# Kernel optimization log

Hardware: AMD Instinct MI355X
Metric: run time of the kernel (lower is better)

Reference implementation:

```python
import jax, jax.numpy as jnp
import numpy as np

B, S = 4, 1024
D_MODEL, N_HEADS, D_SPACE = 1024, 16, 128
N_QK, N_V, N_KNOW = 4096, 4096, 8192
NC_QK, NC_V, NC_KNOW = 64, 64, 64
KC_QK, KC_V, KC_KNOW = 8, 8, 8
MAX_K = 128


def _unit_rows(key, shape):
    w = jax.random.normal(key, shape, jnp.float32)
    return w / (jnp.linalg.norm(w, axis=-1, keepdims=True) + 1e-8)


def setup_inputs() -> dict:
    key = jax.random.key(0)
    ks = jax.random.split(key, 16)
    sd = 0.02
    return {
        "x": jax.random.normal(ks[0], (B, S, D_MODEL), jnp.float32),
        "neuron_emb": jax.random.normal(ks[1], (N_QK + N_V + N_KNOW, D_SPACE), jnp.float32) * sd,
        "proj_attn_k": jax.random.normal(ks[2], (D_MODEL, 3 * D_SPACE), jnp.float32) * sd,
        "proj_attn_b": jnp.zeros((3 * D_SPACE,), jnp.float32),
        "tau_attn_k": jax.random.normal(ks[3], (D_MODEL, 3), jnp.float32) * sd,
        "tau_attn_b": jnp.zeros((3,), jnp.float32),
        "proj_know_k": jax.random.normal(ks[4], (D_MODEL, D_SPACE), jnp.float32) * sd,
        "proj_know_b": jnp.zeros((D_SPACE,), jnp.float32),
        "tau_know_k": jax.random.normal(ks[5], (D_MODEL, 1), jnp.float32) * sd,
        "tau_know_b": jnp.zeros((1,), jnp.float32),
        "cluster_emb_qk": jax.random.normal(ks[6], (NC_QK, D_SPACE), jnp.float32) * sd,
        "cluster_emb_v": jax.random.normal(ks[7], (NC_V, D_SPACE), jnp.float32) * sd,
        "cluster_emb_know": jax.random.normal(ks[8], (NC_KNOW, D_SPACE), jnp.float32) * sd,
        "qk_neurons": _unit_rows(ks[9], (N_QK, D_MODEL)),
        "v_neurons": _unit_rows(ks[10], (N_V, D_MODEL)),
        "know_neurons": _unit_rows(ks[11], (N_KNOW, D_MODEL)),
        "expand_O": jax.random.normal(ks[12], (D_MODEL, D_MODEL), jnp.float32) * sd,
        "ln1_scale": jnp.ones((D_MODEL,), jnp.float32),
        "ln1_bias": jnp.zeros((D_MODEL,), jnp.float32),
        "ln2_scale": jnp.ones((D_MODEL,), jnp.float32),
        "ln2_bias": jnp.zeros((D_MODEL,), jnp.float32),
    }


def _layer_norm(x, scale, bias, eps=1e-6):
    mean = jnp.mean(x, axis=-1, keepdims=True)
    var = jnp.mean(jnp.square(x - mean), axis=-1, keepdims=True)
    return (x - mean) / jnp.sqrt(var + eps) * scale + bias


@jax.checkpoint
def sense_emit(x, neurons, gates):
    # x:[B,S,D] neurons:[N,D] gates:[B,S,N] -> [B,S,D]
    activations = jnp.einsum('bsd,nd->bsn', x, neurons)
    return jnp.einsum('bsn,nd->bsd', activations * gates, neurons)


def threshold_gate(scores, tau, max_k):
    raw_gate = scores - tau
    gate = jnp.where(raw_gate > 0, raw_gate, 1e-8 * jnp.exp(raw_gate))
    exp_gate = jnp.exp(gate) - 1.0
    topk_vals, _ = jax.lax.top_k(exp_gate, max_k)
    threshold = topk_vals[:, :, -1:]
    exp_gate = jnp.where(exp_gate >= threshold, exp_gate, 0.0)
    gate_sum = exp_gate.sum(axis=-1, keepdims=True) + 1e-8
    gate_strength = jnp.tanh(exp_gate.max(axis=-1, keepdims=True))
    return exp_gate / gate_sum * gate_strength


def hierarchical_gate(h, neuron_emb, cluster_emb, tau, n_neurons, n_clusters, k_cluster, max_k):
    Bb, Ss, _ = h.shape
    cluster_size = n_neurons // n_clusters
    ce = cluster_emb / (jnp.linalg.norm(cluster_emb, axis=-1, keepdims=True) + 1e-8)
    cluster_scores = jnp.einsum('bsd,cd->bsc', h, ce)
    _, topk_ids = jax.lax.top_k(cluster_scores, k_cluster)
    cluster_probs = jax.nn.softmax(cluster_scores, axis=-1)
    cluster_freq = cluster_probs.mean(axis=(0, 1))
    cluster_aux = ((cluster_freq - 1.0 / n_clusters) ** 2).sum() * n_clusters
    active_ids = (topk_ids * cluster_size)[:, :, :, None] + jnp.arange(cluster_size)[None, None, None, :]
    active_ids = active_ids.reshape(Bb, Ss, k_cluster * cluster_size)
    active_emb = neuron_emb[active_ids]  # [B,S,A,d_space]
    active_scores = jnp.einsum('bsd,bsnd->bsn', h, active_emb)
    active_gates = threshold_gate(active_scores, tau, max_k)
    gates = jnp.zeros((Bb, Ss, n_neurons), active_gates.dtype)
    bi = jnp.arange(Bb)[:, None, None]
    si = jnp.arange(Ss)[None, :, None]
    gates = gates.at[bi, si, active_ids].set(active_gates)
    neuron_freq = gates.mean(axis=(0, 1))
    neuron_aux = ((neuron_freq - 1.0 / n_neurons) ** 2).sum() * n_neurons
    return gates, cluster_aux, neuron_aux


def _forward(x, neuron_emb, proj_attn_k, proj_attn_b, tau_attn_k, tau_attn_b,
             proj_know_k, proj_know_b, tau_know_k, tau_know_b,
             cluster_emb_qk, cluster_emb_v, cluster_emb_know,
             qk_neurons, v_neurons, know_neurons, expand_O,
             ln1_scale, ln1_bias, ln2_scale, ln2_bias):
    emb_norm = neuron_emb / (jnp.linalg.norm(neuron_emb, axis=-1, keepdims=True) + 1e-8)
    qk_emb = emb_norm[:N_QK]
    v_emb = emb_norm[N_QK:N_QK + N_V]
    know_emb = emb_norm[N_QK + N_V:]

    # --- attention circuit (pre-LN) ---
    h1 = _layer_norm(x, ln1_scale, ln1_bias)
    h_all = h1 @ proj_attn_k + proj_attn_b
    h_Q, h_K, h_V = jnp.split(h_all, 3, axis=-1)
    tau_all = h1 @ tau_attn_k + tau_attn_b
    gate_Q, cq, nq = hierarchical_gate(h_Q, qk_emb, cluster_emb_qk, tau_all[:, :, 0:1], N_QK, NC_QK, KC_QK, MAX_K)
    gate_K, ck, nk = hierarchical_gate(h_K, qk_emb, cluster_emb_qk, tau_all[:, :, 1:2], N_QK, NC_QK, KC_QK, MAX_K)
    gate_V, cv, nv = hierarchical_gate(h_V, v_emb, cluster_emb_v, tau_all[:, :, 2:3], N_V, NC_V, KC_V, MAX_K)
    aux = cq + ck + cv + nq + nk + nv

    Q = sense_emit(h1, qk_neurons, gate_Q)
    K = sense_emit(h1, qk_neurons, gate_K)
    V = sense_emit(h1, v_neurons, gate_V)
    d_head = D_MODEL // N_HEADS
    Q = Q.reshape(B, S, N_HEADS, d_head).transpose(0, 2, 1, 3)
    K = K.reshape(B, S, N_HEADS, d_head).transpose(0, 2, 1, 3)
    V = V.reshape(B, S, N_HEADS, d_head).transpose(0, 2, 1, 3)
    scores = jnp.einsum('bhsd,bhtd->bhst', Q, K) / jnp.sqrt(jnp.float32(d_head))
    causal = jnp.tril(jnp.ones((S, S), dtype=jnp.bool_))
    scores = jnp.where(causal, scores, jnp.finfo(scores.dtype).min)
    attn_w = jax.nn.softmax(scores, axis=-1)
    attn_out = jnp.einsum('bhst,bhtd->bhsd', attn_w, V)
    attn_out = attn_out.transpose(0, 2, 1, 3).reshape(B, S, D_MODEL) @ expand_O
    x = x + attn_out

    # --- knowledge circuit (pre-LN) ---
    h2 = _layer_norm(x, ln2_scale, ln2_bias)
    h_know = h2 @ proj_know_k + proj_know_b
    tau_know = h2 @ tau_know_k + tau_know_b
    gate_know, caux_k2, naux_k2 = hierarchical_gate(h_know, know_emb, cluster_emb_know, tau_know, N_KNOW, NC_KNOW, KC_KNOW, MAX_K)
    aux = aux + caux_k2 + naux_k2
    know_out = sense_emit(h2, know_neurons, gate_know)
    x = x + know_out
    return x, aux


def reference(x, neuron_emb, proj_attn_k, proj_attn_b, tau_attn_k, tau_attn_b,
              proj_know_k, proj_know_b, tau_know_k, tau_know_b,
              cluster_emb_qk, cluster_emb_v, cluster_emb_know,
              qk_neurons, v_neurons, know_neurons, expand_O,
              ln1_scale, ln1_bias, ln2_scale, ln2_bias):
    return _forward(x, neuron_emb, proj_attn_k, proj_attn_b, tau_attn_k, tau_attn_b,
                    proj_know_k, proj_know_b, tau_know_k, tau_know_b,
                    cluster_emb_qk, cluster_emb_v, cluster_emb_know,
                    qk_neurons, v_neurons, know_neurons, expand_O,
                    ln1_scale, ln1_bias, ln2_scale, ln2_bias)
```

## Files before the change

### kernel.cpp

```cpp
#include <hip/hip_runtime.h>

typedef unsigned short u16;
typedef unsigned int u32;
typedef unsigned long long u64;
typedef __attribute__((ext_vector_type(8))) short s16x8;
typedef __attribute__((ext_vector_type(4))) float f32x4;
typedef __attribute__((ext_vector_type(16))) float f32x16;

#define NTOK 4096
#define CAP 144

#define MFMA32(a,b,c) __builtin_amdgcn_mfma_f32_32x32x16_bf16(a,b,c,0,0,0)
#define MFMA16(a,b,c) __builtin_amdgcn_mfma_f32_16x16x32_bf16(a,b,c,0,0,0)

union U16x8 { uint4 u; u16 s[8]; };
union Dw4 { u32 d[4]; s16x8 v; };

__device__ __forceinline__ u16 f2bf(float f) {
    u32 u = __float_as_uint(f);
    u32 r = u + 0x7FFFu + ((u >> 16) & 1u);
    return (u16)(r >> 16);
}
__device__ __forceinline__ u32 pkbf(float lo, float hi) {
    u32 r;
    asm("v_cvt_pk_bf16_f32 %0, %1, %2" : "=v"(r) : "v"(lo), "v"(hi));
    return r;
}
__device__ __forceinline__ u32 mapkey(float f) {
    u32 b = __float_as_uint(f);
    return (b & 0x80000000u) ? ~b : (b | 0x80000000u);
}

__global__ __launch_bounds__(256) void norm_rows_kernel(const float* __restrict__ in,
                                                        u16* __restrict__ out16,
                                                        float* __restrict__ outRow, int rows)
{
    int row = blockIdx.x * 4 + (threadIdx.x >> 6);
    int lane = threadIdx.x & 63;
    if (row >= rows) return;
    float2 v = *(const float2*)&in[(size_t)row * 128 + lane * 2];
    float ss = v.x * v.x + v.y * v.y;
    #pragma unroll
    for (int o = 1; o < 64; o <<= 1) ss += __shfl_xor(ss, o);
    float rn = 1.0f / (sqrtf(ss) + 1e-8f);
    float2 ov = make_float2(v.x * rn, v.y * rn);
    if (out16)
        *(u32*)&out16[(size_t)row * 128 + lane * 2] = pkbf(ov.x, ov.y);
    if (outRow)
        *(float2*)&outRow[(size_t)row * 128 + lane * 2] = ov;
}

__global__ __launch_bounds__(256) void cast_bf16_kernel(const float* __restrict__ in,
                                                        u16* __restrict__ out, int n)
{
    int i = (blockIdx.x * 256 + threadIdx.x) * 4;
    if (i >= n) return;
    float4 v = *(const float4*)&in[i];
    ushort4 o;
    o.x = f2bf(v.x); o.y = f2bf(v.y); o.z = f2bf(v.z); o.w = f2bf(v.w);
    *(ushort4*)&out[i] = o;
}

__global__ __launch_bounds__(256) void cast_gateh_kernel(const float* __restrict__ h, int stride,
                                                         int ngates, u16* __restrict__ out)
{
    int t = blockIdx.x, tid = threadIdx.x;
    int total = ngates * 128;
    for (int i = tid; i < total; i += 256) {
        int g = i >> 7, d = i & 127;
        out[(size_t)g * NTOK * 128 + (size_t)t * 128 + d] = f2bf(h[(size_t)t * stride + i]);
    }
}

__global__ void transpose_cast_kernel(const float* __restrict__ in, u16* __restrict__ out,
                                      int Nn, int Kk)
{
    __shared__ float sT[64][65];
    int n0 = blockIdx.x * 64, k0 = blockIdx.y * 64;
    int tx = threadIdx.x, ty = threadIdx.y;
    #pragma unroll
    for (int r = 0; r < 64; r += 4)
        sT[ty + r][tx] = in[(size_t)(k0 + ty + r) * Nn + n0 + tx];
    __syncthreads();
    #pragma unroll
    for (int r = 0; r < 64; r += 4)
        out[(size_t)(n0 + ty + r) * Kk + k0 + tx] = f2bf(sT[tx][ty + r]);
}

__global__ void ntab_transpose_kernel(const u16* __restrict__ in, u16* __restrict__ out, int NCLv)
{
    __shared__ u16 tile[64][65];
    int cc = blockIdx.x, db = blockIdx.y * 64, jb = blockIdx.z * 64;
    int tx = threadIdx.x, ty = threadIdx.y;
    const u16* src = in + (size_t)cc * NCLv * 1024;
    #pragma unroll
    for (int r = 0; r < 64; r += 4)
        tile[ty + r][tx] = src[(size_t)(jb + ty + r) * 1024 + db + tx];
    __syncthreads();
    u16* dst = out + (size_t)cc * NCLv * 1024;
    #pragma unroll
    for (int r = 0; r < 64; r += 4)
        dst[(size_t)(db + ty + r) * NCLv + jb + tx] = tile[tx][ty + r];
}

__global__ __launch_bounds__(256) void ln_kernel(const float* __restrict__ x,
                                                 const float* __restrict__ gam,
                                                 const float* __restrict__ bet,
                                                 float* __restrict__ out,
                                                 u16* __restrict__ outbf)
{
    __shared__ float red[8];
    int t = blockIdx.x, tid = threadIdx.x;
    const float* row = x + (size_t)t * 1024;
    float4 v = *(const float4*)&row[tid * 4];
    float s = v.x + v.y + v.z + v.w;
    #pragma unroll
    for (int o = 1; o < 64; o <<= 1) s += __shfl_xor(s, o);
    if ((tid & 63) == 0) red[tid >> 6] = s;
    __syncthreads();
    float mean = (red[0] + red[1] + red[2] + red[3]) * (1.0f / 1024.0f);
    float d0 = v.x - mean, d1 = v.y - mean, d2 = v.z - mean, d3 = v.w - mean;
    float ss = d0 * d0 + d1 * d1 + d2 * d2 + d3 * d3;
    #pragma unroll
    for (int o = 1; o < 64; o <<= 1) ss += __shfl_xor(ss, o);
    if ((tid & 63) == 0) red[4 + (tid >> 6)] = ss;
    __syncthreads();
    float var = (red[4] + red[5] + red[6] + red[7]) * (1.0f / 1024.0f);
    float rstd = 1.0f / sqrtf(var + 1e-6f);
    int d = tid * 4;
    float4 g4 = *(const float4*)&gam[d];
    float4 b4 = *(const float4*)&bet[d];
    float4 o4;
    o4.x = d0 * rstd * g4.x + b4.x;
    o4.y = d1 * rstd * g4.y + b4.y;
    o4.z = d2 * rstd * g4.z + b4.z;
    o4.w = d3 * rstd * g4.w + b4.w;
    *(float4*)&out[(size_t)t * 1024 + d] = o4;
    if (outbf) {
        ushort4 ob;
        ob.x = f2bf(o4.x); ob.y = f2bf(o4.y); ob.z = f2bf(o4.z); ob.w = f2bf(o4.w);
        *(ushort4*)&outbf[(size_t)t * 1024 + d] = ob;
    }
}

__global__ __launch_bounds__(256) void gemm_mfma_kernel(const u16* __restrict__ A,
                                                        const u16* __restrict__ Bt,
                                                        const float* __restrict__ bias,
                                                        const float* __restrict__ resid,
                                                        float* __restrict__ C, int N, int K)
{
    __shared__ __align__(16) u16 sA[128 * 80];
    __shared__ __align__(16) u16 sB[128 * 80];
    int n0 = blockIdx.x * 128, m0 = blockIdx.y * 128;
    int tid = threadIdx.x;
    int l = tid & 63, wid = tid >> 6;
    int wm = wid >> 1, wn = wid & 1;
    int l15 = l & 15, hi4 = l >> 4;
    f32x4 acc[4][4];
    #pragma unroll
    for (int i = 0; i < 4; ++i)
        #pragma unroll
        for (int j = 0; j < 4; ++j)
            #pragma unroll
            for (int q = 0; q < 4; ++q) acc[i][j][q] = 0.f;

    int sr = tid >> 1, scb = (tid & 1) * 4;
    for (int k0 = 0; k0 < K; k0 += 64) {
        __syncthreads();
        #pragma unroll
        for (int j = 0; j < 4; ++j) {
            int ch = scb + j;
            uint4 va = *(const uint4*)&A[(size_t)(m0 + sr) * K + k0 + ch * 8];
            *(uint4*)&sA[sr * 80 + ch * 8] = va;
            uint4 vb = *(const uint4*)&Bt[(size_t)(n0 + sr) * K + k0 + ch * 8];
            *(uint4*)&sB[sr * 80 + ch * 8] = vb;
        }
        __syncthreads();
        #pragma unroll
        for (int kc = 0; kc < 2; ++kc) {
            s16x8 af[4], bf[4];
            #pragma unroll
            for (int mf = 0; mf < 4; ++mf)
                af[mf] = *(const s16x8*)&sA[(wm * 64 + mf * 16 + l15) * 80 + kc * 32 + hi4 * 8];
            #pragma unroll
            for (int nf = 0; nf < 4; ++nf)
                bf[nf] = *(const s16x8*)&sB[(wn * 64 + nf * 16 + l15) * 80 + kc * 32 + hi4 * 8];
            #pragma unroll
            for (int mf = 0; mf < 4; ++mf)
                #pragma unroll
                for (int nf = 0; nf < 4; ++nf)
                    acc[mf][nf] = MFMA16(af[mf], bf[nf], acc[mf][nf]);
        }
    }
    #pragma unroll
    for (int mf = 0; mf < 4; ++mf)
        #pragma unroll
        for (int nf = 0; nf < 4; ++nf)
            #pragma unroll
            for (int j = 0; j < 4; ++j) {
                int row = m0 + wm * 64 + mf * 16 + hi4 * 4 + j;
                int col = n0 + wn * 64 + nf * 16 + l15;
                float v = acc[mf][nf][j];
                if (bias) v += bias[col];
                if (resid) v += resid[(size_t)row * N + col];
                C[(size_t)row * N + col] = v;
            }
}

__global__ __launch_bounds__(64) void vecproj_kernel(const float* __restrict__ h,
                                                     const float* __restrict__ W,
                                                     const float* __restrict__ bias,
                                                     float* __restrict__ out, int nw)
{
    int t = blockIdx.x, lane = threadIdx.x;
    float p0 = 0.f, p1 = 0.f, p2 = 0.f;
    #pragma unroll
    for (int it = 0; it < 4; ++it) {
        int d = it * 256 + lane * 4;
        float4 h4 = *(const float4*)&h[(size_t)t * 1024 + d];
        if (nw == 1) {
            float4 w4 = *(const float4*)&W[d];
            p0 += h4.x * w4.x + h4.y * w4.y + h4.z * w4.z + h4.w * w4.w;
        } else {
            float4 w0 = *(const float4*)&W[d * 3];
            float4 w1 = *(const float4*)&W[d * 3 + 4];
            float4 w2 = *(const float4*)&W[d * 3 + 8];
            p0 += h4.x * w0.x + h4.y * w0.w + h4.z * w1.z + h4.w * w2.y;
            p1 += h4.x * w0.y + h4.y * w1.x + h4.z * w1.w + h4.w * w2.z;
            p2 += h4.x * w0.z + h4.y * w1.y + h4.z * w2.x + h4.w * w2.w;
        }
    }
    #pragma unroll
    for (int o = 1; o < 64; o <<= 1) {
        p0 += __shfl_xor(p0, o);
        p1 += __shfl_xor(p1, o);
        p2 += __shfl_xor(p2, o);
    }
    if (lane == 0) {
        out[(size_t)t * nw + 0] = p0 + bias[0];
        if (nw > 1) out[(size_t)t * nw + 1] = p1 + bias[1];
        if (nw > 2) out[(size_t)t * nw + 2] = p2 + bias[2];
    }
}

__global__ __launch_bounds__(256) void cluster_kernel(
    const float* __restrict__ hsrc, int hstride,
    const float* __restrict__ cebase,
    float* __restrict__ cprob, int* __restrict__ topcg, int gate_base)
{
    __shared__ float sH[32 * 136];
    __shared__ float sC[64 * 136];
    int gy = blockIdx.y;
    const float* ce = cebase + (size_t)(gy >> 1) * (64 * 128);
    int hoff = gy * 128;
    int gout = gate_base + gy;
    int t0 = blockIdx.x * 32;
    int tid = threadIdx.x;

    {
        int r = tid >> 3, c0 = (tid & 7) * 16;
        const float* src = hsrc + (size_t)(t0 + r) * hstride + hoff + c0;
        #pragma unroll
        for (int q = 0; q < 16; q += 4)
            *(float4*)&sH[r * 136 + c0 + q] = *(const float4*)&src[q];
    }
    {
        int r = tid >> 2, c0 = (tid & 3) * 32;
        const float* src = ce + (size_t)r * 128 + c0;
        #pragma unroll
        for (int q = 0; q < 32; q += 4)
            *(float4*)&sC[r * 136 + c0 + q] = *(const float4*)&src[q];
    }
    __syncthreads();

    int tt = tid >> 3, cl0 = tid & 7;
    float acc[8] = {};
    for (int d4 = 0; d4 < 128; d4 += 4) {
        float4 hv = *(const float4*)&sH[tt * 136 + d4];
        #pragma unroll
        for (int c8 = 0; c8 < 8; ++c8) {
            float4 cv = *(const float4*)&sC[(cl0 + 8 * c8) * 136 + d4];
            acc[c8] = fmaf(hv.x, cv.x, acc[c8]);
            acc[c8] = fmaf(hv.y, cv.y, acc[c8]);
            acc[c8] = fmaf(hv.z, cv.z, acc[c8]);
            acc[c8] = fmaf(hv.w, cv.w, acc[c8]);
        }
    }
    __syncthreads();
    float* sS = sH;
    #pragma unroll
    for (int c8 = 0; c8 < 8; ++c8)
        sS[tt * 72 + cl0 + 8 * c8] = acc[c8];
    __syncthreads();

    int w = tid >> 6, lane = tid & 63;
    for (int k = 0; k < 8; ++k) {
        int t = w * 8 + k;
        float s = sS[t * 72 + lane];
        float mx = s;
        #pragma unroll
        for (int o = 1; o < 64; o <<= 1) mx = fmaxf(mx, __shfl_xor(mx, o));
        float e = expf(s - mx);
        float sm = e;
        #pragma unroll
        for (int o = 1; o < 64; o <<= 1) sm += __shfl_xor(sm, o);
        cprob[((size_t)gout * NTOK + t0 + t) * 64 + lane] = e / sm;
        int rank = 0;
        for (int j = 0; j < 64; ++j) {
            float sj = sS[t * 72 + j];
            rank += (sj > s || (sj == s && j < lane)) ? 1 : 0;
        }
        if (rank < 8) topcg[((size_t)gout * NTOK + t0 + t) * 8 + rank] = lane;
    }
}

__global__ __launch_bounds__(1024) void listbuild_kernel(
    const int* __restrict__ topc_base, u32* __restrict__ entries_base,
    u32* __restrict__ tiletab_base, int* __restrict__ ntiles_base)
{
    __shared__ int cnt[64], offp[64], woff[64], tbase[64];
    int g = blockIdx.x;
    const int* tc = topc_base + (size_t)g * NTOK * 8;
    u32* eg = entries_base + (size_t)g * 40960;
    u32* tt = tiletab_base + (size_t)g * 640;
    int tid = threadIdx.x;
    if (tid < 64) { cnt[tid] = 0; woff[tid] = 0; }
    __syncthreads();
    int myc[32];
    #pragma unroll
    for (int i = 0; i < 32; ++i) {
        int t = tid * 4 + (i >> 3), s = i & 7;
        int c = tc[(size_t)t * 8 + s] & 63;
        myc[i] = c;
        atomicAdd(&cnt[c], 1);
    }
    __syncthreads();
    if (tid < 64) {
        int pc = (cnt[tid] + 63) & ~63;
        int sum = pc;
        #pragma unroll
        for (int o = 1; o < 64; o <<= 1) { int up = __shfl_up(sum, o); if (tid >= o) sum += up; }
        offp[tid] = sum - pc;
        int nt = pc >> 6;
        int tsum = nt;
        #pragma unroll
        for (int o = 1; o < 64; o <<= 1) { int up = __shfl_up(tsum, o); if (tid >= o) tsum += up; }
        tbase[tid] = tsum - nt;
        if (tid == 63) ntiles_base[g] = tsum;
    }
    __syncthreads();
    int totpad = offp[63] + ((cnt[63] + 63) & ~63);
    for (int i = tid; i < totpad; i += 1024) eg[i] = 0xFFFFFFFFu;
    __syncthreads();
    #pragma unroll
    for (int i = 0; i < 32; ++i) {
        int t = tid * 4 + (i >> 3), s = i & 7;
        int c = myc[i];
        int pos = offp[c] + atomicAdd(&woff[c], 1);
        eg[pos] = (u32)t | ((u32)s << 12);
    }
    __syncthreads();
    if (tid < 64) {
        int nt = ((cnt[tid] + 63) & ~63) >> 6;
        int eb = offp[tid] >> 6;
        for (int k2 = 0; k2 < nt; ++k2)
            tt[tbase[tid] + k2] = ((u32)tid << 16) | (u32)(eb + k2);
    }
}

template<int NCL>
__global__ __launch_bounds__(256) void score_bs_kernel(
    const u16* __restrict__ hgbf,
    const u16* __restrict__ embbase,
    float* __restrict__ scsbase,
    const u32* __restrict__ entries,
    const u32* __restrict__ tiletab,
    const int* __restrict__ ntiles)
{
    constexpr int NFR = NCL / 16;
    __shared__ __align__(16) u16 sH[64 * 136];
    __shared__ __align__(16) u16 sE[NCL * 136];
    __shared__ u32 ent[64];
    int gy = blockIdx.y;
    int bsw = ((int)blockIdx.x & 7) * 80 + ((int)blockIdx.x >> 3);
    if (bsw >= ntiles[gy]) return;
    u32 te = tiletab[(size_t)gy * 640 + bsw];
    int c = (int)(te >> 16) & 63;
    int e0 = (int)(te & 0x3FFu) * 64;
    const u32* eg = entries + (size_t)gy * 40960;
    const u16* Hg = hgbf + (size_t)gy * NTOK * 128;
    const u16* emb = embbase + (size_t)(gy >> 1) * 4096 * 128 + (size_t)c * NCL * 128;
    float* scs = scsbase + (size_t)gy * NTOK * (8 * NCL);

    int tid = threadIdx.x;
    int w = tid >> 6, lane = tid & 63;
    int l15 = lane & 15, hi4 = lane >> 4;

    if (tid < 64) ent[tid] = eg[e0 + tid];
    __syncthreads();

    #pragma unroll
    for (int u = 0; u < 4; ++u) {
        int idx = tid + u * 256;
        int r = idx >> 4, cq = idx & 15;
        int t = (int)(ent[r] & 4095u);
        uint4 v = *(const uint4*)&Hg[(size_t)t * 128 + cq * 8];
        *(uint4*)&sH[r * 136 + cq * 8] = v;
    }
    #pragma unroll
    for (int u = 0; u < NCL / 16; ++u) {
        int idx = tid + u * 256;
        int r = idx >> 4, cq = idx & 15;
        uint4 v = *(const uint4*)&emb[(size_t)r * 128 + cq * 8];
        *(uint4*)&sE[r * 136 + cq * 8] = v;
    }
    __syncthreads();

    f32x4 acc[NFR];
    #pragma unroll
    for (int nf = 0; nf < NFR; ++nf) { acc[nf][0] = 0.f; acc[nf][1] = 0.f; acc[nf][2] = 0.f; acc[nf][3] = 0.f; }
    #pragma unroll
    for (int kc = 0; kc < 4; ++kc) {
        s16x8 af = *(const s16x8*)&sH[(w * 16 + l15) * 136 + kc * 32 + hi4 * 8];
        #pragma unroll
        for (int nf = 0; nf < NFR; ++nf) {
            s16x8 bf = *(const s16x8*)&sE[(nf * 16 + l15) * 136 + kc * 32 + hi4 * 8];
            acc[nf] = MFMA16(af, bf, acc[nf]);
        }
    }

    int row0 = w * 16 + hi4 * 4;
    #pragma unroll
    for (int jj = 0; jj < 4; ++jj) {
        u32 e = ent[row0 + jj];
        if (e != 0xFFFFFFFFu) {
            int t = (int)(e & 4095u), s = (int)((e >> 12) & 7u);
            float* orow = scs + (size_t)t * (8 * NCL) + s * NCL;
            #pragma unroll
            for (int nf = 0; nf < NFR; ++nf)
                orow[nf * 16 + l15] = acc[nf][jj];
        }
    }
}

template<int NCAND, int LGCS>
__global__ __launch_bounds__(256) void gate_select_kernel(
    float* __restrict__ scsg,
    const float* __restrict__ tausrc, int taustride,
    const int* __restrict__ topcg,
    int* __restrict__ gidx, float* __restrict__ gval, int* __restrict__ gcnt,
    int gate_base)
{
    constexpr int CSM = (1 << LGCS) - 1;
    __shared__ float lds_scs[4][NCAND];
    __shared__ int   lds_hist[4][256];
    __shared__ int   lds_topc[4][8];
    __shared__ float lds_keg[4][CAP];

    int gy = blockIdx.y;
    int gg = gate_base + gy;
    int tauoff = gy;
    const int* tsrc = topcg + (size_t)gg * NTOK * 8;
    float* scs = scsg + (size_t)gy * NTOK * NCAND;
    gidx += (size_t)gg * NTOK * CAP;
    gval += (size_t)gg * NTOK * CAP;
    gcnt += gg * NTOK;

    int w = threadIdx.x >> 6, lane = threadIdx.x & 63;
    int t = blockIdx.x * 4 + w;

    float* srow = scs + (size_t)t * NCAND;
    #pragma unroll
    for (int c0 = 0; c0 < NCAND; c0 += 64)
        lds_scs[w][c0 + lane] = srow[c0 + lane];
    if (lane < 8) lds_topc[w][lane] = tsrc[(size_t)t * 8 + lane] & 63;

    unsigned prefix = 0; int k = 128;
    #pragma unroll
    for (int shift = 24; shift >= 0; shift -= 8) {
        lds_hist[w][lane] = 0;
        lds_hist[w][lane + 64] = 0;
        lds_hist[w][lane + 128] = 0;
        lds_hist[w][lane + 192] = 0;
        unsigned mhi = (shift == 24) ? 0u : (0xFFFFFFFFu << (shift + 8));
        #pragma unroll
        for (int ii = 0; ii < NCAND; ii += 64) {
            unsigned key = mapkey(lds_scs[w][ii + lane]);
            if ((key & mhi) == prefix) atomicAdd(&lds_hist[w][(key >> shift) & 255], 1);
        }
        int s0 = lds_hist[w][4 * lane], s1 = lds_hist[w][4 * lane + 1];
        int s2 = lds_hist[w][4 * lane + 2], s3 = lds_hist[w][4 * lane + 3];
        int sl = s0 + s1 + s2 + s3;
        int suf = sl;
        #pragma unroll
        for (int o = 1; o < 64; o <<= 1) {
            int ov = __shfl_down(suf, o);
            if (lane + o < 64) suf += ov;
        }
        int run = suf - sl;
        int seld = -1, selk = 0;
        if (run < k && k <= run + s3) { seld = 4 * lane + 3; selk = k - run; }
        run += s3;
        if (seld < 0 && run < k && k <= run + s2) { seld = 4 * lane + 2; selk = k - run; }
        run += s2;
        if (seld < 0 && run < k && k <= run + s1) { seld = 4 * lane + 1; selk = k - run; }
        run += s1;
        if (seld < 0 && run < k && k <= run + s0) { seld = 4 * lane + 0; selk = k - run; }
        u64 mk = __ballot(seld >= 0);
        int owner = __ffsll(mk) - 1;
        int sd = __shfl(seld, owner);
        k = __shfl(selk, owner);
        prefix |= ((unsigned)sd) << shift;
    }
    unsigned thrkey = prefix;

    float tau = tausrc[(size_t)t * taustride + tauoff];
    int basec = 0;
    float lsum = 0.f, lmaxs = -3.0e38f;
    #pragma unroll
    for (int c0 = 0; c0 < NCAND; c0 += 64) {
        float s = lds_scs[w][c0 + lane];
        lmaxs = fmaxf(lmaxs, s);
        bool pred = (mapkey(s) >= thrkey);
        float eg = 0.f;
        if (pred) {
            float raw = s - tau;
            float g2 = raw > 0.f ? raw : 1e-8f * expf(raw);
            eg = expf(g2) - 1.0f;
            lsum += eg;
        }
        u64 mk = __ballot(pred);
        int pos = basec + __popcll(mk & ((1ull << lane) - 1ull));
        if (pred && pos < CAP) {
            lds_hist[w][pos] = c0 + lane;
            lds_keg[w][pos] = eg;
        }
        basec += __popcll(mk);
    }
    #pragma unroll
    for (int o = 1; o < 64; o <<= 1) {
        lsum += __shfl_xor(lsum, o);
        lmaxs = fmaxf(lmaxs, __shfl_xor(lmaxs, o));
    }
    float rawm = lmaxs - tau;
    float gm = rawm > 0.f ? rawm : 1e-8f * expf(rawm);
    float egm = expf(gm) - 1.0f;
    float scalev = tanhf(egm) / (lsum + 1e-8f);
    int nkept = basec < CAP ? basec : CAP;

    for (int p = lane; p < nkept; p += 64) {
        int i = lds_hist[w][p];
        float eg = lds_keg[w][p];
        int neuron = (lds_topc[w][i >> LGCS] << LGCS) + (i & CSM);
        gidx[(size_t)t * CAP + p] = neuron;
        gval[(size_t)t * CAP + p] = eg * scalev;
    }
    if (lane == 0) gcnt[t] = nkept;

    #pragma unroll
    for (int c0 = 0; c0 < NCAND; c0 += 64) {
        int i = c0 + lane;
        float s = lds_scs[w][i];
        float wv = 0.f;
        if (mapkey(s) >= thrkey) {
            float raw = s - tau;
            float g2 = raw > 0.f ? raw : 1e-8f * expf(raw);
            wv = (expf(g2) - 1.0f) * scalev;
        }
        srow[i] = wv;
    }
}

template<int NCL>
__global__ __launch_bounds__(256) void sense_bs_kernel(
    const u16* __restrict__ hbf,
    const u16* __restrict__ ntab,
    const u16* __restrict__ ntabT,
    const float* __restrict__ Wg,
    const u32* __restrict__ entries,
    const u32* __restrict__ tiletab,
    const int* __restrict__ ntiles,
    u16* __restrict__ partial)
{
    constexpr int NTP = NCL + 8;
    constexpr int NFR = NCL / 16;
    constexpr int LQ = (NCL == 64) ? 3 : 4;
    __shared__ __align__(16) char smem[(64 + NCL) * 144 + NCL * 128 + 256];
    u16* sH = (u16*)smem;
    u16* sN = (u16*)(smem + 64 * 144);
    u16* sNT = (u16*)smem;
    u16* sP = (u16*)(smem + (64 + NCL) * 144);
    u32* ent = (u32*)(smem + (64 + NCL) * 144 + NCL * 128);

    int bsw = ((int)blockIdx.x & 7) * 80 + ((int)blockIdx.x >> 3);
    if (bsw >= *ntiles) return;
    u32 te = tiletab[bsw];
    int c = (int)(te >> 16) & 63;
    int e0 = (int)(te & 0x3FFu) * 64;

    int tid = threadIdx.x;
    int w = tid >> 6, lane = tid & 63;
    int l15 = lane & 15, hi4 = lane >> 4;

    if (tid < 64) ent[tid] = entries[e0 + tid];
    __syncthreads();

    const u16* nbase = ntab + (size_t)c * NCL * 1024;
    const u16* ntT = ntabT + (size_t)c * NCL * 1024;

    f32x4 acc[NFR];
    #pragma unroll
    for (int nf = 0; nf < NFR; ++nf) { acc[nf][0] = 0.f; acc[nf][1] = 0.f; acc[nf][2] = 0.f; acc[nf][3] = 0.f; }

    for (int k0 = 0; k0 < 1024; k0 += 64) {
        __syncthreads();
        #pragma unroll
        for (int u = 0; u < 2; ++u) {
            int idx = tid + u * 256;
            int r = idx >> 3, cq = idx & 7;
            int t = (int)(ent[r] & 4095u);
            uint4 v = *(const uint4*)&hbf[(size_t)t * 1024 + k0 + cq * 8];
            *(uint4*)&sH[r * 72 + cq * 8] = v;
        }
        #pragma unroll
        for (int u = 0; u < NCL / 32; ++u) {
            int idx = tid + u * 256;
            int r = idx >> 3, cq = idx & 7;
            uint4 v = *(const uint4*)&nbase[(size_t)r * 1024 + k0 + cq * 8];
            *(uint4*)&sN[r * 72 + cq * 8] = v;
        }
        __syncthreads();
        #pragma unroll
        for (int kc = 0; kc < 2; ++kc) {
            s16x8 af = *(const s16x8*)&sH[(w * 16 + l15) * 72 + kc * 32 + hi4 * 8];
            #pragma unroll
            for (int nf = 0; nf < NFR; ++nf) {
                s16x8 bf = *(const s16x8*)&sN[(nf * 16 + l15) * 72 + kc * 32 + hi4 * 8];
                acc[nf] = MFMA16(af, bf, acc[nf]);
            }
        }
    }
    __syncthreads();

    int row0 = w * 16 + hi4 * 4;
    u32 erow[4]; bool evalid[4];
    #pragma unroll
    for (int jj = 0; jj < 4; ++jj) { erow[jj] = ent[row0 + jj]; evalid[jj] = (erow[jj] != 0xFFFFFFFFu); }
    #pragma unroll
    for (int jj = 0; jj < 4; ++jj) {
        int t = (int)(erow[jj] & 4095u), s = (int)((erow[jj] >> 12) & 7u);
        const float* wrow = Wg + (size_t)t * (8 * NCL) + s * NCL;
        #pragma unroll
        for (int nf = 0; nf < NFR; ++nf) {
            float wv = wrow[nf * 16 + l15];
            sP[(row0 + jj) * NCL + nf * 16 + l15] = f2bf(acc[nf][jj] * wv);
        }
    }
    __syncthreads();

    for (int dch = 0; dch < 16; ++dch) {
        int d0 = dch * 64;
        __syncthreads();
        #pragma unroll
        for (int u = 0; u < NCL / 32; ++u) {
            int v = tid + u * 256;
            int dr = v >> LQ, jq = v & ((1 << LQ) - 1);
            uint4 t4 = *(const uint4*)&ntT[(size_t)(d0 + dr) * NCL + jq * 8];
            *(uint4*)&sNT[dr * NTP + jq * 8] = t4;
        }
        __syncthreads();
        f32x4 ab[4];
        #pragma unroll
        for (int df = 0; df < 4; ++df) { ab[df][0] = 0.f; ab[df][1] = 0.f; ab[df][2] = 0.f; ab[df][3] = 0.f; }
        #pragma unroll
        for (int kc = 0; kc < NCL / 32; ++kc) {
            s16x8 af = *(const s16x8*)&sP[(w * 16 + l15) * NCL + kc * 32 + hi4 * 8];
            #pragma unroll
            for (int df = 0; df < 4; ++df) {
                s16x8 bf = *(const s16x8*)&sNT[(df * 16 + l15) * NTP + kc * 32 + hi4 * 8];
                ab[df] = MFMA16(af, bf, ab[df]);
            }
        }
        #pragma unroll
        for (int jj = 0; jj < 4; ++jj) {
            if (evalid[jj]) {
                int t = (int)(erow[jj] & 4095u), s = (int)((erow[jj] >> 12) & 7u);
                u16* prow = partial + ((size_t)t * 8 + s) * 1024 + d0;
                #pragma unroll
                for (int df = 0; df < 4; ++df)
                    prow[df * 16 + l15] = f2bf(ab[df][jj]);
            }
        }
    }
}

__global__ __launch_bounds__(256) void slot_reduce_kernel(
    const u16* __restrict__ partial, u16* __restrict__ outq, float* __restrict__ outadd)
{
    int t = blockIdx.x, tid = threadIdx.x;
    int d0 = tid * 4;
    float s0 = 0.f, s1 = 0.f, s2 = 0.f, s3 = 0.f;
    #pragma unroll
    for (int s = 0; s < 8; ++s) {
        ushort4 u = *(const ushort4*)&partial[((size_t)t * 8 + s) * 1024 + d0];
        s0 += __uint_as_float((u32)u.x << 16);
        s1 += __uint_as_float((u32)u.y << 16);
        s2 += __uint_as_float((u32)u.z << 16);
        s3 += __uint_as_float((u32)u.w << 16);
    }
    if (outq) {
        int b = t >> 10, st = t & 1023;
        int head = d0 >> 6, dh = d0 & 63;
        ushort4 o;
        o.x = f2bf(s0); o.y = f2bf(s1); o.z = f2bf(s2); o.w = f2bf(s3);
        *(ushort4*)&outq[(((size_t)b * 16 + head) * 1024 + st) * 64 + dh] = o;
    } else {
        float* op = outadd + (size_t)t * 1024 + d0;
        float4 cur = *(const float4*)op;
        cur.x += s0; cur.y += s1; cur.z += s2; cur.w += s3;
        *(float4*)op = cur;
    }
}

__global__ __launch_bounds__(256) void nfreq_partial_kernel(
    const int* __restrict__ gidx, const float* __restrict__ gval,
    const int* __restrict__ gcnt, const float* __restrict__ cprob,
    float* __restrict__ partials, float* __restrict__ cpart2)
{
    __shared__ float hist[8192];
    __shared__ float csum[4][64];
    int slice = blockIdx.x, gate = blockIdx.y;
    int N = (gate == 3) ? 8192 : 4096;
    int tid = threadIdx.x;
    int w = tid >> 6, lane = tid & 63;
    for (int i = tid; i < N; i += 256) hist[i] = 0.f;

    {
        const float* cp = cprob + (size_t)gate * NTOK * 64;
        float cs = 0.f;
        #pragma unroll
        for (int i = 0; i < 16; ++i) {
            int t = slice * 64 + i * 4 + w;
            cs += cp[(size_t)t * 64 + lane];
        }
        csum[w][lane] = cs;
    }
    __syncthreads();

    const int* gi = gidx + (size_t)gate * NTOK * CAP;
    const float* gv = gval + (size_t)gate * NTOK * CAP;
    const int* gc = gcnt + gate * NTOK;
    #pragma unroll 4
    for (int i = 0; i < 16; ++i) {
        int t = slice * 64 + i * 4 + w;
        int cnt = gc[t];
        for (int p = lane; p < cnt; p += 64) {
            int n = gi[(size_t)t * CAP + p];
            float v = gv[(size_t)t * CAP + p];
            atomicAdd(&hist[n], v);
        }
    }
    __syncthreads();
    float* op = partials + ((size_t)gate * 64 + slice) * 8192;
    for (int i = tid; i < N; i += 256) op[i] = hist[i];
    if (tid < 64)
        cpart2[((size_t)gate * 64 + slice) * 64 + tid] =
            csum[0][tid] + csum[1][tid] + csum[2][tid] + csum[3][tid];
}

__global__ __launch_bounds__(256) void aux2_kernel(const float* __restrict__ partials,
                                                   const float* __restrict__ cpart2,
                                                   float* __restrict__ outp)
{
    __shared__ float red[4];
    __shared__ float cred[4][64];
    int bid = blockIdx.x, tid = threadIdx.x;
    float local = 0.f;
    if (bid < 80) {
        int gn = bid * 256 + tid;
        int gate = (gn < 12288) ? (gn >> 12) : 3;
        int ln = (gn < 12288) ? (gn & 4095) : (gn - 12288);
        const float* base = partials + (size_t)gate * 64 * 8192 + ln;
        float s = 0.f;
        #pragma unroll 8
        for (int c = 0; c < 64; ++c) s += base[(size_t)c * 8192];
        float Nf = (gate == 3) ? 8192.f : 4096.f;
        float f = s * (1.0f / 4096.0f);
        float d = f - 1.0f / Nf;
        local = d * d * Nf;
    } else {
        int gate = bid - 80;
        int w = tid >> 6, lane = tid & 63;
        const float* base = cpart2 + (size_t)gate * 64 * 64;
        float s = 0.f;
        #pragma unroll
        for (int i = 0; i < 16; ++i) s += base[(size_t)(i * 4 + w) * 64 + lane];
        cred[w][lane] = s;
        __syncthreads();
        if (tid < 64) {
            float tot = cred[0][tid] + cred[1][tid] + cred[2][tid] + cred[3][tid];
            float f = tot * (1.0f / 4096.0f);
            float d = f - (1.0f / 64.0f);
            local = d * d * 64.0f;
        }
    }
    #pragma unroll
    for (int o = 1; o < 64; o <<= 1) local += __shfl_xor(local, o);
    if ((tid & 63) == 0) red[tid >> 6] = local;
    __syncthreads();
    if (tid == 0) atomicAdd(outp, red[0] + red[1] + red[2] + red[3]);
}

__global__ __launch_bounds__(256) void attn_kernel(const u16* __restrict__ Qb,
                                                   const u16* __restrict__ Kb,
                                                   const u16* __restrict__ Vb,
                                                   u16* __restrict__ outbf)
{
    __shared__ __align__(16) u32 VT[2048];
    __shared__ float csh[128];
    __shared__ float lsh[128];
    int qt = blockIdx.x;
    int bh = blockIdx.y;
    int b = bh >> 4, hh = bh & 15;
    int tid = threadIdx.x;
    int w = tid >> 6, lane = tid & 63;
    int hi = lane >> 5, l31 = lane & 31;
    int qb = qt * 128;
    int qcol = qb + w * 32 + l31;
    int wqmax = qb + w * 32 + 31;
    int ktmax = 2 * qt + 1;

    const u16* Qbase = Qb + (size_t)bh * 1024 * 64;
    const u16* Kbase = Kb + (size_t)bh * 1024 * 64;
    const u16* Vbase = Vb + (size_t)bh * 1024 * 64;

    s16x8 qf[4];
    #pragma unroll
    for (int c = 0; c < 4; ++c)
        qf[c] = *(const s16x8*)&Qbase[(size_t)qcol * 64 + c * 16 + hi * 8];

    int vkey = 2 * (tid & 31);
    int vd = (tid >> 5) * 8;
    uint4 va  = *(const uint4*)&Vbase[(size_t)vkey * 64 + vd];
    uint4 vb2 = *(const uint4*)&Vbase[(size_t)(vkey + 1) * 64 + vd];

    s16x8 kf[2][4];
    #pragma unroll
    for (int s = 0; s < 2; ++s)
        #pragma unroll
        for (int c = 0; c < 4; ++c)
            kf[s][c] = *(const s16x8*)&Kbase[(size_t)(s * 32 + l31) * 64 + c * 16 + hi * 8];

    float m = -3.0e38f, lden = 0.f;
    f32x16 oacc0, oacc1;
    #pragma unroll
    for (int r = 0; r < 16; ++r) { oacc0[r] = 0.f; oacc1[r] = 0.f; }

    for (int kt = 0; kt <= ktmax; ++kt) {
        __syncthreads();
        {
            U16x8 ua, ub; ua.u = va; ub.u = vb2;
            #pragma unroll
            for (int j = 0; j < 8; ++j) {
                int d = vd + j;
                u32 pk = (u32)ua.s[j] | ((u32)ub.s[j] << 16);
                VT[(u32)((d * 32 + (tid & 31)) ^ ((d & 7) << 2))] = pk;
            }
        }
        __syncthreads();

        bool active = (kt * 64) <= wqmax;
        f32x16 s0, s1;
        if (active) {
            #pragma unroll
            for (int r = 0; r < 16; ++r) { s0[r] = 0.f; s1[r] = 0.f; }
            #pragma unroll
            for (int c = 0; c < 4; ++c) {
                s0 = MFMA32(kf[0][c], qf[c], s0);
                s1 = MFMA32(kf[1][c], qf[c], s1);
            }
        }
        if (kt < ktmax) {
            int nb = (kt + 1) * 64;
            va  = *(const uint4*)&Vbase[(size_t)(nb + vkey) * 64 + vd];
            vb2 = *(const uint4*)&Vbase[(size_t)(nb + vkey + 1) * 64 + vd];
            if (nb <= wqmax) {
                #pragma unroll
                for (int s = 0; s < 2; ++s)
                    #pragma unroll
                    for (int c = 0; c < 4; ++c)
                        kf[s][c] = *(const s16x8*)&Kbase[(size_t)(nb + s * 32 + l31) * 64 + c * 16 + hi * 8];
            }
        }
        if (active) {
            float p0[16], p1[16];
            float pmax = -3.0e38f;
            #pragma unroll
            for (int r = 0; r < 16; ++r) {
                int crow = (r & 3) + 8 * (r >> 2) + 4 * hi;
                int k0 = kt * 64 + crow;
                float v0 = (k0 <= qcol) ? s0[r] * 0.125f : -3.0e38f;
                float v1 = (k0 + 32 <= qcol) ? s1[r] * 0.125f : -3.0e38f;
                p0[r] = v0; p1[r] = v1;
                pmax = fmaxf(pmax, fmaxf(v0, v1));
            }
            pmax = fmaxf(pmax, __shfl_xor(pmax, 32));
            float mn = fmaxf(m, pmax);
            float corr = __expf(m - mn);
            float rs = 0.f;
            #pragma unroll
            for (int r = 0; r < 16; ++r) {
                p0[r] = __expf(p0[r] - mn);
                p1[r] = __expf(p1[r] - mn);
                rs += p0[r] + p1[r];
            }
            rs += __shfl_xor(rs, 32);
            lden = lden * corr + rs;
            m = mn;
            if (hi == 0) csh[w * 32 + l31] = corr;
            float c16[16];
            #pragma unroll
            for (int r = 0; r < 16; ++r)
                c16[r] = csh[w * 32 + ((r & 3) + 8 * (r >> 2) + 4 * hi)];
            #pragma unroll
            for (int r = 0; r < 16; ++r) { oacc0[r] *= c16[r]; oacc1[r] *= c16[r]; }

            #pragma unroll
            for (int sub = 0; sub < 2; ++sub) {
                u32 e[8], x[8];
                #pragma unroll
                for (int j = 0; j < 8; ++j) {
                    float lo = sub ? p1[2 * j] : p0[2 * j];
                    float hi2 = sub ? p1[2 * j + 1] : p0[2 * j + 1];
                    e[j] = pkbf(lo, hi2);
                }
                #pragma unroll
                for (int j = 0; j < 8; ++j) x[j] = (u32)__shfl_xor((int)e[j], 32);
                Dw4 t0, t1;
                t0.d[0] = hi ? x[2] : e[0];
                t0.d[1] = hi ? x[3] : e[1];
                t0.d[2] = hi ? e[2] : x[0];
                t0.d[3] = hi ? e[3] : x[1];
                t1.d[0] = hi ? x[6] : e[4];
                t1.d[1] = hi ? x[7] : e[5];
                t1.d[2] = hi ? e[6] : x[4];
                t1.d[3] = hi ? e[7] : x[5];
                int kb0 = sub * 32 + hi * 8;
                int kb1 = kb0 + 16;
                int d0 = l31, d1 = 32 + l31;
                const char* vtb = (const char*)VT;
                s16x8 vf;
                vf = *(const s16x8*)(vtb + (((d0 * 128 + kb0 * 2)) ^ ((d0 & 7) << 4)));
                oacc0 = MFMA32(t0.v, vf, oacc0);
                vf = *(const s16x8*)(vtb + (((d1 * 128 + kb0 * 2)) ^ ((d1 & 7) << 4)));
                oacc1 = MFMA32(t0.v, vf, oacc1);
                vf = *(const s16x8*)(vtb + (((d0 * 128 + kb1 * 2)) ^ ((d0 & 7) << 4)));
                oacc0 = MFMA32(t1.v, vf, oacc0);
                vf = *(const s16x8*)(vtb + (((d1 * 128 + kb1 * 2)) ^ ((d1 & 7) << 4)));
                oacc1 = MFMA32(t1.v, vf, oacc1);
            }
        }
    }
    if (hi == 0) lsh[w * 32 + l31] = 1.0f / lden;
    float li[16];
    #pragma unroll
    for (int r = 0; r < 16; ++r)
        li[r] = lsh[w * 32 + ((r & 3) + 8 * (r >> 2) + 4 * hi)];
    #pragma unroll
    for (int r = 0; r < 16; ++r) {
        int crow = (r & 3) + 8 * (r >> 2) + 4 * hi;
        size_t token = (size_t)b * 1024 + qb + w * 32 + crow;
        outbf[token * 1024 + hh * 64 + l31]      = f2bf(oacc0[r] * li[r]);
        outbf[token * 1024 + hh * 64 + 32 + l31] = f2bf(oacc1[r] * li[r]);
    }
}

extern "C" void kernel_launch(void* const* d_in, const int* in_sizes, int n_in,
                              void* d_out, int out_size, void* d_ws, size_t ws_size,
                              hipStream_t stream) {
    const float* x            = (const float*)d_in[0];
    const float* neuron_emb   = (const float*)d_in[1];
    const float* proj_attn_k  = (const float*)d_in[2];
    const float* proj_attn_b  = (const float*)d_in[3];
    const float* tau_attn_k   = (const float*)d_in[4];
    const float* tau_attn_b   = (const float*)d_in[5];
    const float* proj_know_k  = (const float*)d_in[6];
    const float* proj_know_b  = (const float*)d_in[7];
    const float* tau_know_k   = (const float*)d_in[8];
    const float* tau_know_b   = (const float*)d_in[9];
    const float* cluster_qk   = (const float*)d_in[10];
    const float* cluster_v    = (const float*)d_in[11];
    const float* cluster_know = (const float*)d_in[12];
    const float* qk_neurons   = (const float*)d_in[13];
    const float* v_neurons    = (const float*)d_in[14];
    const float* know_neurons = (const float*)d_in[15];
    const float* expand_O     = (const float*)d_in[16];
    const float* ln1_s        = (const float*)d_in[17];
    const float* ln1_b        = (const float*)d_in[18];
    const float* ln2_s        = (const float*)d_in[19];
    const float* ln2_b        = (const float*)d_in[20];
    float* out = (float*)d_out;

    char* wsb = (char*)d_ws;
    size_t off = 0;
    auto alloc = [&](size_t bytes) -> void* {
        void* p = wsb + off;
        off = (off + bytes + 255) & ~(size_t)255;
        return p;
    };
    u16*   emb16    = (u16*)alloc((size_t)16384 * 128 * 2);
    float* ce_norm  = (float*)alloc((size_t)3 * 64 * 128 * 4);
    u16*   nbf      = (u16*)alloc((size_t)16384 * 1024 * 2);
    float* h1       = (float*)alloc((size_t)NTOK * 1024 * 4);
    u16*   h1bf     = (u16*)alloc((size_t)NTOK * 1024 * 2);
    float* h_all    = (float*)alloc((size_t)NTOK * 384 * 4);
    float* tau_all  = (float*)alloc((size_t)NTOK * 3 * 4);
    u16*   hgbf     = (u16*)alloc((size_t)4 * NTOK * 128 * 2);
    int*   gidx     = (int*)alloc((size_t)4 * NTOK * CAP * 4);
    float* gvalp    = (float*)alloc((size_t)4 * NTOK * CAP * 4);
    int*   gcnt     = (int*)alloc((size_t)4 * NTOK * 4);
    int*   topcg    = (int*)alloc((size_t)4 * NTOK * 8 * 4);
    float* Wattn    = (float*)alloc((size_t)3 * NTOK * 512 * 4);
    u32*   entries  = (u32*)alloc((size_t)4 * 40960 * 4);
    u32*   tiletab  = (u32*)alloc((size_t)4 * 640 * 4);
    int*   ntiles   = (int*)alloc((size_t)4 * 4);
    u16*   qkv      = (u16*)alloc((size_t)3 * NTOK * 1024 * 2);
    u16*   projA_t  = (u16*)alloc((size_t)384 * 1024 * 2);
    u16*   know_t   = (u16*)alloc((size_t)128 * 1024 * 2);
    u16*   exp_t    = (u16*)alloc((size_t)1024 * 1024 * 2);
    float* cprob    = (float*)alloc((size_t)4 * NTOK * 64 * 4);
    float* cpart2   = (float*)alloc((size_t)4 * 64 * 64 * 4);
    u16*   spartial = (u16*)alloc((size_t)NTOK * 8 * 1024 * 2);

    float* h_know   = h_all;
    float* tau_kn   = tau_all;
    float* Wknow    = Wattn;
    float* partials = Wattn + (size_t)NTOK * 1024;
    u16* ntT_qk   = (u16*)h1;
    u16* ntT_v    = (u16*)h1 + (size_t)4096 * 1024;
    u16* ntT_know = (u16*)h1;

    u16* Qbuf = qkv;
    u16* Kbuf = qkv + (size_t)NTOK * 1024;
    u16* Vbuf = qkv + (size_t)2 * NTOK * 1024;
    u16* attn_bf = h1bf;

    hipMemsetAsync(out + (size_t)NTOK * 1024, 0, 4, stream);

    norm_rows_kernel<<<16384 / 4, 256, 0, stream>>>(neuron_emb, emb16, nullptr, 16384);
    norm_rows_kernel<<<16, 256, 0, stream>>>(cluster_qk, nullptr, ce_norm, 64);
    norm_rows_kernel<<<16, 256, 0, stream>>>(cluster_v, nullptr, ce_norm + 64 * 128, 64);
    norm_rows_kernel<<<16, 256, 0, stream>>>(cluster_know, nullptr, ce_norm + 2 * 64 * 128, 64);
    cast_bf16_kernel<<<4096, 256, 0, stream>>>(qk_neurons, nbf, 4096 * 1024);
    cast_bf16_kernel<<<4096, 256, 0, stream>>>(v_neurons, nbf + (size_t)4096 * 1024, 4096 * 1024);
    cast_bf16_kernel<<<8192, 256, 0, stream>>>(know_neurons, nbf + (size_t)8192 * 1024, 8192 * 1024);
    transpose_cast_kernel<<<dim3(6, 16), dim3(64, 4), 0, stream>>>(proj_attn_k, projA_t, 384, 1024);
    transpose_cast_kernel<<<dim3(2, 16), dim3(64, 4), 0, stream>>>(proj_know_k, know_t, 128, 1024);
    transpose_cast_kernel<<<dim3(16, 16), dim3(64, 4), 0, stream>>>(expand_O, exp_t, 1024, 1024);

    ln_kernel<<<NTOK, 256, 0, stream>>>(x, ln1_s, ln1_b, h1, h1bf);
    gemm_mfma_kernel<<<dim3(3, 32), 256, 0, stream>>>(h1bf, projA_t, proj_attn_b, nullptr, h_all, 384, 1024);
    vecproj_kernel<<<NTOK, 64, 0, stream>>>(h1, tau_attn_k, tau_attn_b, tau_all, 3);
    ntab_transpose_kernel<<<dim3(64, 16, 1), dim3(64, 4), 0, stream>>>(nbf, ntT_qk, 64);
    ntab_transpose_kernel<<<dim3(64, 16, 1), dim3(64, 4), 0, stream>>>(
        nbf + (size_t)4096 * 1024, ntT_v, 64);

    cluster_kernel<<<dim3(NTOK / 32, 3), 256, 0, stream>>>(h_all, 384, ce_norm, cprob, topcg, 0);
    listbuild_kernel<<<3, 1024, 0, stream>>>(topcg, entries, tiletab, ntiles);
    cast_gateh_kernel<<<NTOK, 256, 0, stream>>>(h_all, 384, 3, hgbf);
    score_bs_kernel<64><<<dim3(640, 3), 256, 0, stream>>>(hgbf, emb16, Wattn, entries, tiletab, ntiles);
    gate_select_kernel<512, 6><<<dim3(1024, 3), 256, 0, stream>>>(
        Wattn, tau_all, 3, topcg, gidx, gvalp, gcnt, 0);

    for (int g = 0; g < 3; ++g) {
        const u16* tab  = nbf + (g == 2 ? (size_t)4096 * 1024 : 0);
        const u16* tabT = (g == 2) ? ntT_v : ntT_qk;
        sense_bs_kernel<64><<<640, 256, 0, stream>>>(
            h1bf, tab, tabT, Wattn + (size_t)g * NTOK * 512,
            entries + (size_t)g * 40960, tiletab + (size_t)g * 640, ntiles + g, spartial);
        u16* outq = (g == 0) ? Qbuf : (g == 1) ? Kbuf : Vbuf;
        slot_reduce_kernel<<<NTOK, 256, 0, stream>>>(spartial, outq, nullptr);
    }

    attn_kernel<<<dim3(8, 64), 256, 0, stream>>>(Qbuf, Kbuf, Vbuf, attn_bf);
    gemm_mfma_kernel<<<dim3(8, 32), 256, 0, stream>>>(attn_bf, exp_t, nullptr, x, out, 1024, 1024);

    ln_kernel<<<NTOK, 256, 0, stream>>>(out, ln2_s, ln2_b, h1, h1bf);
    gemm_mfma_kernel<<<dim3(1, 32), 256, 0, stream>>>(h1bf, know_t, proj_know_b, nullptr, h_know, 128, 1024);
    vecproj_kernel<<<NTOK, 64, 0, stream>>>(h1, tau_know_k, tau_know_b, tau_kn, 1);
    ntab_transpose_kernel<<<dim3(64, 16, 2), dim3(64, 4), 0, stream>>>(
        nbf + (size_t)8192 * 1024, ntT_know, 128);

    cluster_kernel<<<dim3(NTOK / 32, 1), 256, 0, stream>>>(h_know, 128, ce_norm + 2 * 64 * 128,
                                                           cprob, topcg, 3);
    listbuild_kernel<<<1, 1024, 0, stream>>>(topcg + (size_t)3 * NTOK * 8,
                                             entries + (size_t)3 * 40960,
                                             tiletab + (size_t)3 * 640, ntiles + 3);
    cast_gateh_kernel<<<NTOK, 256, 0, stream>>>(h_know, 128, 1, hgbf + (size_t)3 * NTOK * 128);
    score_bs_kernel<128><<<dim3(640, 1), 256, 0, stream>>>(
        hgbf + (size_t)3 * NTOK * 128, emb16 + (size_t)8192 * 128, Wknow,
        entries + (size_t)3 * 40960, tiletab + (size_t)3 * 640, ntiles + 3);
    gate_select_kernel<1024, 7><<<dim3(1024, 1), 256, 0, stream>>>(
        Wknow, tau_kn, 1, topcg, gidx, gvalp, gcnt, 3);
    sense_bs_kernel<128><<<640, 256, 0, stream>>>(
        h1bf, nbf + (size_t)8192 * 1024, ntT_know, Wknow,
        entries + (size_t)3 * 40960, tiletab + (size_t)3 * 640, ntiles + 3, spartial);
    slot_reduce_kernel<<<NTOK, 256, 0, stream>>>(spartial, nullptr, out);

    nfreq_partial_kernel<<<dim3(64, 4), 256, 0, stream>>>(gidx, gvalp, gcnt, cprob, partials, cpart2);
    aux2_kernel<<<84, 256, 0, stream>>>(partials, cpart2, out + (size_t)NTOK * 1024);
}
```

Measured before the change: 735.5 us.

## Split causal attention over two KV halves and merge partial softmax results

The attention kernel now splits each query tile's causal key range into two equal halves, one per blockIdx.z, doubling the grid from 512 to 1024 blocks. Each half writes unnormalised bf16 partial outputs plus running max and denominator, and a new merge kernel combines them with log-sum-exp weights. This targets low occupancy and the load imbalance of the causal diagonal on a machine with many CUs. In exchange it adds partial-buffer traffic, an extra launch, and some precision loss because partials are rounded to bf16 before merging.

```diff
diff --git a/kernel.cpp b/kernel.cpp
--- a/kernel.cpp
+++ b/kernel.cpp
@@ -21,6 +21,7 @@
     u32 r = u + 0x7FFFu + ((u >> 16) & 1u);
     return (u16)(r >> 16);
 }
+__device__ __forceinline__ float bf2f(u16 v) { return __uint_as_float((u32)v << 16); }
 __device__ __forceinline__ u32 pkbf(float lo, float hi) {
     u32 r;
     asm("v_cvt_pk_bf16_f32 %0, %1, %2" : "=v"(r) : "v"(lo), "v"(hi));
@@ -811,24 +812,25 @@
     if (tid == 0) atomicAdd(outp, red[0] + red[1] + red[2] + red[3]);
 }
 
-__global__ __launch_bounds__(256) void attn_kernel(const u16* __restrict__ Qb,
-                                                   const u16* __restrict__ Kb,
-                                                   const u16* __restrict__ Vb,
-                                                   u16* __restrict__ outbf)
+__global__ __launch_bounds__(256) void attn_split_kernel(const u16* __restrict__ Qb,
+                                                         const u16* __restrict__ Kb,
+                                                         const u16* __restrict__ Vb,
+                                                         u16* __restrict__ Opart,
+                                                         float2* __restrict__ mlb)
 {
     __shared__ __align__(16) u32 VT[2048];
     __shared__ float csh[128];
-    __shared__ float lsh[128];
     int qt = blockIdx.x;
     int bh = blockIdx.y;
-    int b = bh >> 4, hh = bh & 15;
+    int z = blockIdx.z;
     int tid = threadIdx.x;
     int w = tid >> 6, lane = tid & 63;
     int hi = lane >> 5, l31 = lane & 31;
     int qb = qt * 128;
     int qcol = qb + w * 32 + l31;
     int wqmax = qb + w * 32 + 31;
-    int ktmax = 2 * qt + 1;
+    int kt0 = z * (qt + 1);
+    int kt1 = kt0 + (qt + 1);
 
     const u16* Qbase = Qb + (size_t)bh * 1024 * 64;
     const u16* Kbase = Kb + (size_t)bh * 1024 * 64;
@@ -841,22 +843,23 @@
 
     int vkey = 2 * (tid & 31);
     int vd = (tid >> 5) * 8;
-    uint4 va  = *(const uint4*)&Vbase[(size_t)vkey * 64 + vd];
-    uint4 vb2 = *(const uint4*)&Vbase[(size_t)(vkey + 1) * 64 + vd];
+    int base0 = kt0 * 64;
+    uint4 va  = *(const uint4*)&Vbase[(size_t)(base0 + vkey) * 64 + vd];
+    uint4 vb2 = *(const uint4*)&Vbase[(size_t)(base0 + vkey + 1) * 64 + vd];
 
     s16x8 kf[2][4];
     #pragma unroll
     for (int s = 0; s < 2; ++s)
         #pragma unroll
         for (int c = 0; c < 4; ++c)
-            kf[s][c] = *(const s16x8*)&Kbase[(size_t)(s * 32 + l31) * 64 + c * 16 + hi * 8];
+            kf[s][c] = *(const s16x8*)&Kbase[(size_t)(base0 + s * 32 + l31) * 64 + c * 16 + hi * 8];
 
     float m = -3.0e38f, lden = 0.f;
     f32x16 oacc0, oacc1;
     #pragma unroll
     for (int r = 0; r < 16; ++r) { oacc0[r] = 0.f; oacc1[r] = 0.f; }
 
-    for (int kt = 0; kt <= ktmax; ++kt) {
+    for (int kt = kt0; kt < kt1; ++kt) {
         __syncthreads();
         {
             U16x8 ua, ub; ua.u = va; ub.u = vb2;
@@ -880,7 +883,7 @@
                 s1 = MFMA32(kf[1][c], qf[c], s1);
             }
         }
-        if (kt < ktmax) {
+        if (kt + 1 < kt1) {
             int nb = (kt + 1) * 64;
             va  = *(const uint4*)&Vbase[(size_t)(nb + vkey) * 64 + vd];
             vb2 = *(const uint4*)&Vbase[(size_t)(nb + vkey + 1) * 64 + vd];
@@ -961,18 +964,42 @@
             }
         }
     }
-    if (hi == 0) lsh[w * 32 + l31] = 1.0f / lden;
-    float li[16];
-    #pragma unroll
-    for (int r = 0; r < 16; ++r)
-        li[r] = lsh[w * 32 + ((r & 3) + 8 * (r >> 2) + 4 * hi)];
+    size_t pi = (size_t)(z * 8 + qt) * 64 + bh;
+    if (hi == 0)
+        mlb[pi * 128 + w * 32 + l31] = make_float2(m, lden);
     #pragma unroll
     for (int r = 0; r < 16; ++r) {
         int crow = (r & 3) + 8 * (r >> 2) + 4 * hi;
-        size_t token = (size_t)b * 1024 + qb + w * 32 + crow;
-        outbf[token * 1024 + hh * 64 + l31]      = f2bf(oacc0[r] * li[r]);
-        outbf[token * 1024 + hh * 64 + 32 + l31] = f2bf(oacc1[r] * li[r]);
-    }
+        u16* orow = Opart + (pi * 128 + w * 32 + crow) * 64;
+        orow[l31]      = f2bf(oacc0[r]);
+        orow[32 + l31] = f2bf(oacc1[r]);
+    }
+}
+
+__global__ __launch_bounds__(256) void attn_merge_kernel(const u16* __restrict__ Opart,
+                                                         const float2* __restrict__ mlb,
+                                                         u16* __restrict__ outbf)
+{
+    int t = blockIdx.x, tid = threadIdx.x;
+    int b = t >> 10, s = t & 1023;
+    int qt = s >> 7, qrow = s & 127;
+    int hh = tid >> 4, q4 = (tid & 15) * 4;
+    size_t pi0 = (size_t)qt * 64 + (b * 16 + hh);
+    size_t pi1 = (size_t)(8 + qt) * 64 + (b * 16 + hh);
+    float2 ml0 = mlb[pi0 * 128 + qrow];
+    float2 ml1 = mlb[pi1 * 128 + qrow];
+    float M = fmaxf(ml0.x, ml1.x);
+    float w0 = __expf(ml0.x - M);
+    float w1 = __expf(ml1.x - M);
+    float inv = 1.0f / (ml0.y * w0 + ml1.y * w1);
+    ushort4 a = *(const ushort4*)&Opart[(pi0 * 128 + qrow) * 64 + q4];
+    ushort4 c = *(const ushort4*)&Opart[(pi1 * 128 + qrow) * 64 + q4];
+    ushort4 o;
+    o.x = f2bf((bf2f(a.x) * w0 + bf2f(c.x) * w1) * inv);
+    o.y = f2bf((bf2f(a.y) * w0 + bf2f(c.y) * w1) * inv);
+    o.z = f2bf((bf2f(a.z) * w0 + bf2f(c.z) * w1) * inv);
+    o.w = f2bf((bf2f(a.w) * w0 + bf2f(c.w) * w1) * inv);
+    *(ushort4*)&outbf[(size_t)t * 1024 + hh * 64 + q4] = o;
 }
 
 extern "C" void kernel_launch(void* const* d_in, const int* in_sizes, int n_in,
@@ -1031,6 +1058,8 @@
     float* cprob    = (float*)alloc((size_t)4 * NTOK * 64 * 4);
     float* cpart2   = (float*)alloc((size_t)4 * 64 * 64 * 4);
     u16*   spartial = (u16*)alloc((size_t)NTOK * 8 * 1024 * 2);
+    u16*   Opart    = (u16*)alloc((size_t)2 * 8 * 64 * 128 * 64 * 2);
+    float2* mlb     = (float2*)alloc((size_t)2 * 8 * 64 * 128 * 8);
 
     float* h_know   = h_all;
     float* tau_kn   = tau_all;
@@ -1082,7 +1111,8 @@
         slot_reduce_kernel<<<NTOK, 256, 0, stream>>>(spartial, outq, nullptr);
     }
 
-    attn_kernel<<<dim3(8, 64), 256, 0, stream>>>(Qbuf, Kbuf, Vbuf, attn_bf);
+    attn_split_kernel<<<dim3(8, 64, 2), 256, 0, stream>>>(Qbuf, Kbuf, Vbuf, Opart, mlb);
+    attn_merge_kernel<<<NTOK, 256, 0, stream>>>(Opart, mlb, attn_bf);
     gemm_mfma_kernel<<<dim3(8, 32), 256, 0, stream>>>(attn_bf, exp_t, nullptr, x, out, 1024, 1024);
 
     ln_kernel<<<NTOK, 256, 0, stream>>>(out, ln2_s, ln2_b, h1, h1bf);
```

Result: faster. 715.5 us (-2.7%).
